# Kernel optimization log

Hardware: AMD Instinct MI355X
Metric: run time of the kernel (lower is better)

## Reference

```python
import jax, jax.numpy as jnp
import numpy as np

N_HEAD = 4
TOP_K = 16


def _layernorm(x, g, b, eps=1e-5):
    mu = jnp.mean(x, axis=-1, keepdims=True)
    var = jnp.var(x, axis=-1, keepdims=True)
    return (x - mu) * jax.lax.rsqrt(var + eps) * g + b


def _gelu_new(x):
    c = np.sqrt(2.0 / np.pi).astype(np.float32)
    return 0.5 * x * (1.0 + jnp.tanh(c * (x + 0.044715 * x ** 3)))


def _l2_normalize(x, eps=1e-12):
    n = jnp.sqrt(jnp.sum(x * x, axis=1, keepdims=True))
    return x / jnp.maximum(n, eps)


def setup_inputs() -> dict:
    key = jax.random.key(0)
    ks = jax.random.split(key, 16)
    B, S, DIN, D, L, P, N = 128, 64, 6, 128, 3, 24, 500000
    sd = 0.02
    inp = {
        "x": jax.random.normal(ks[0], (B, S, DIN), jnp.float32),
        "memory_keys": _l2_normalize(jax.random.normal(ks[1], (N, D), jnp.float32)),
        "memory_values": jax.random.normal(ks[2], (N, P, DIN), jnp.float32),
        "wpe": sd * jax.random.normal(ks[3], (S, D), jnp.float32),
        "w_in": sd * jax.random.normal(ks[4], (DIN, D), jnp.float32),
        "b_in": jnp.zeros((D,), jnp.float32),
        "ln1_g": jnp.ones((L, D), jnp.float32),
        "ln1_b": jnp.zeros((L, D), jnp.float32),
        "attn_w": sd * jax.random.normal(ks[5], (L, D, 3 * D), jnp.float32),
        "attn_b": jnp.zeros((L, 3 * D), jnp.float32),
        "attn_pw": sd * jax.random.normal(ks[6], (L, D, D), jnp.float32),
        "attn_pb": jnp.zeros((L, D), jnp.float32),
        "ln2_g": jnp.ones((L, D), jnp.float32),
        "ln2_b": jnp.zeros((L, D), jnp.float32),
        "fc_w": sd * jax.random.normal(ks[7], (L, D, 4 * D), jnp.float32),
        "fc_b": jnp.zeros((L, 4 * D), jnp.float32),
        "mlp_pw": sd * jax.random.normal(ks[8], (L, 4 * D, D), jnp.float32),
        "mlp_pb": jnp.zeros((L, D), jnp.float32),
        "lnf_g": jnp.ones((D,), jnp.float32),
        "lnf_b": jnp.zeros((D,), jnp.float32),
        "w_out": sd * jax.random.normal(ks[9], (S * D, P * DIN), jnp.float32),
        "b_out": jnp.zeros((P * DIN,), jnp.float32),
        "ret_w1": sd * jax.random.normal(ks[10], (DIN, D), jnp.float32),
        "ret_b1": jnp.zeros((D,), jnp.float32),
        "ret_w2": sd * jax.random.normal(ks[11], (S * D, D), jnp.float32),
        "ret_b2": jnp.zeros((D,), jnp.float32),
        "fusion_weight": jnp.float32(0.5),
    }
    return inp


def _forward(x, memory_keys, memory_values, wpe, w_in, b_in, ln1_g, ln1_b,
             attn_w, attn_b, attn_pw, attn_pb, ln2_g, ln2_b, fc_w, fc_b,
             mlp_pw, mlp_pb, lnf_g, lnf_b, w_out, b_out, ret_w1, ret_b1,
             ret_w2, ret_b2, fusion_weight):
    B, S, DIN = x.shape
    D = w_in.shape[1]
    L = attn_w.shape[0]
    P = memory_values.shape[1]
    hd = D // N_HEAD
    # GPT2 backbone with inputs_embeds (eval mode: dropout = identity)
    h = x @ w_in + b_in + wpe[:S]
    causal = jnp.tril(jnp.ones((S, S), bool))
    neg = jnp.finfo(h.dtype).min
    for l in range(L):
        a = _layernorm(h, ln1_g[l], ln1_b[l])
        qkv = a @ attn_w[l] + attn_b[l]                       # [B,S,3D]
        q, k, v = jnp.split(qkv, 3, axis=-1)
        q = q.reshape(B, S, N_HEAD, hd).transpose(0, 2, 1, 3)  # bhsd
        k = k.reshape(B, S, N_HEAD, hd).transpose(0, 2, 1, 3)
        v = v.reshape(B, S, N_HEAD, hd).transpose(0, 2, 1, 3)
        scores = jnp.einsum('bhqd,bhkd->bhqk', q, k) / np.sqrt(hd).astype(np.float32)
        scores = jnp.where(causal, scores, neg)
        att = jax.nn.softmax(scores, axis=-1)
        o = jnp.einsum('bhqk,bhkd->bhqd', att, v)
        o = o.transpose(0, 2, 1, 3).reshape(B, S, D)
        h = h + o @ attn_pw[l] + attn_pb[l]
        m = _layernorm(h, ln2_g[l], ln2_b[l])
        h = h + _gelu_new(m @ fc_w[l] + fc_b[l]) @ mlp_pw[l] + mlp_pb[l]
    h = _layernorm(h, lnf_g, lnf_b)
    base_pred = (h.reshape(B, S * D) @ w_out + b_out).reshape(B, P, DIN)
    # Retrieval branch: encode query, cosine sim against memory, top-k gather
    q_emb = (x @ ret_w1 + ret_b1).reshape(B, S * D) @ ret_w2 + ret_b2
    q_emb = _l2_normalize(q_emb)
    sim = q_emb @ memory_keys.T                               # [B,N] (memory-bound)
    topk_sim, topk_idx = jax.lax.top_k(sim, TOP_K)
    weights = jax.nn.softmax(topk_sim, axis=1)                # [B,K]
    vals = memory_values[topk_idx]                            # [B,K,P,DIN] gather
    retrieved = jnp.einsum('bk,bkpd->bpd', weights, vals)
    alpha = jax.nn.sigmoid(fusion_weight)
    return alpha * base_pred + (1.0 - alpha) * retrieved


def reference(x, memory_keys, memory_values, wpe, w_in, b_in, ln1_g, ln1_b,
              attn_w, attn_b, attn_pw, attn_pb, ln2_g, ln2_b, fc_w, fc_b,
              mlp_pw, mlp_pb, lnf_g, lnf_b, w_out, b_out, ret_w1, ret_b1,
              ret_w2, ret_b2, fusion_weight):
    return _forward(x, memory_keys, memory_values, wpe, w_in, b_in, ln1_g, ln1_b,
                    attn_w, attn_b, attn_pw, attn_pb, ln2_g, ln2_b, fc_w, fc_b,
                    mlp_pw, mlp_pb, lnf_g, lnf_b, w_out, b_out, ret_w1, ret_b1,
                    ret_w2, ret_b2, fusion_weight)
```

## Files before the change

kernel.cpp:

```cpp
#include <hip/hip_runtime.h>
#include <math.h>

#define TOK   8192
#define DM    128
#define NKEY  500000
#define PDIM  144
#define KSPLIT 128

#define SB     512
#define NPASS  7813
#define NCAND  (SB * 16)

typedef __attribute__((ext_vector_type(8))) short short8;
typedef __attribute__((ext_vector_type(4))) float f32x4;

__device__ __forceinline__ short f2bf(float x) {
    union { float f; unsigned u; } v; v.f = x;
    unsigned r = v.u + 0x7FFFu + ((v.u >> 16) & 1u);
    return (short)(r >> 16);
}
__device__ __forceinline__ float bf2f(short h) {
    union { float f; unsigned u; } v;
    v.u = ((unsigned)(unsigned short)h) << 16;
    return v.f;
}

__device__ __forceinline__ void ins16(float v, int id, float* tv, int* tix) {
#pragma unroll
    for (int j = 15; j > 0; j--) {
        bool up = v > tv[j];
        bool sh = v > tv[j - 1];
        float nv = sh ? tv[j - 1] : v;
        int   ni = sh ? tix[j - 1] : id;
        tv[j]  = up ? nv : tv[j];
        tix[j] = up ? ni : tix[j];
    }
    if (v > tv[0]) { tv[0] = v; tix[0] = id; }
}

__global__ __launch_bounds__(256) void k_embed2(
    const float* __restrict__ x, const float* __restrict__ w,
    const float* __restrict__ b, const float* __restrict__ wpe,
    float* __restrict__ out, const float* __restrict__ rw,
    const float* __restrict__ rb, float* __restrict__ rout)
{
    int bid = blockIdx.x;
    if (bid < 4096) {
        int idx = bid * 256 + threadIdx.x;
        int t = idx >> 7, d = idx & 127;
        float acc = b[d] + wpe[(t & 63) * DM + d];
        const float* xr = x + t * 6;
#pragma unroll
        for (int i = 0; i < 6; i++) acc = fmaf(xr[i], w[i * DM + d], acc);
        out[idx] = acc;
    } else {
        int idx = (bid - 4096) * 256 + threadIdx.x;
        int t = idx >> 7, d = idx & 127;
        float acc = rb[d];
        const float* xr = x + t * 6;
#pragma unroll
        for (int i = 0; i < 6; i++) acc = fmaf(xr[i], rw[i * DM + d], acc);
        rout[idx] = acc;
    }
}

__global__ __launch_bounds__(256) void k_ln(
    const float* __restrict__ in, const float* __restrict__ g,
    const float* __restrict__ b, float* __restrict__ out)
{
    int row = blockIdx.x * 4 + (threadIdx.x >> 6);
    int lane = threadIdx.x & 63;
    const float* r = in + row * DM;
    float v0 = r[lane], v1 = r[lane + 64];
    float s = v0 + v1, ss = v0 * v0 + v1 * v1;
#pragma unroll
    for (int o = 32; o; o >>= 1) { s += __shfl_down(s, o); ss += __shfl_down(ss, o); }
    s = __shfl(s, 0); ss = __shfl(ss, 0);
    float mean = s * (1.f / 128.f);
    float var = ss * (1.f / 128.f) - mean * mean;
    float rstd = rsqrtf(var + 1e-5f);
    out[row * DM + lane]      = (v0 - mean) * rstd * g[lane]      + b[lane];
    out[row * DM + lane + 64] = (v1 - mean) * rstd * g[lane + 64] + b[lane + 64];
}

template<int ACT>
__global__ __launch_bounds__(256) void k_gemmln(
    const float* __restrict__ A, const float* __restrict__ g,
    const float* __restrict__ bln, const float* __restrict__ W,
    const float* __restrict__ bias, float* __restrict__ C, int NC)
{
    __shared__ float As[128][68];
    __shared__ float Ws[16][68];
    const int tid = threadIdx.x;
    const int m0 = blockIdx.x * 64, n0 = blockIdx.y * 64;
    {
        int row = tid >> 2, part = tid & 3;
        const float* ar = A + (long)(m0 + row) * 128 + part * 32;
        float v[32];
        float s = 0.f, ss = 0.f;
#pragma unroll
        for (int i2 = 0; i2 < 8; i2++) {
            float4 t = *(const float4*)(ar + i2 * 4);
            v[i2 * 4 + 0] = t.x; v[i2 * 4 + 1] = t.y;
            v[i2 * 4 + 2] = t.z; v[i2 * 4 + 3] = t.w;
            s += t.x + t.y + t.z + t.w;
            ss += t.x * t.x + t.y * t.y + t.z * t.z + t.w * t.w;
        }
        s += __shfl_xor(s, 1); s += __shfl_xor(s, 2);
        ss += __shfl_xor(ss, 1); ss += __shfl_xor(ss, 2);
        float mean = s * (1.f / 128.f);
        float rstd = rsqrtf(ss * (1.f / 128.f) - mean * mean + 1e-5f);
#pragma unroll
        for (int i = 0; i < 32; i++) {
            int d = part * 32 + i;
            As[d][row] = (v[i] - mean) * rstd * g[d] + bln[d];
        }
    }
    const int ty = tid >> 4, tx = tid & 15;
    float acc[4][4];
#pragma unroll
    for (int i = 0; i < 4; i++)
#pragma unroll
        for (int j = 0; j < 4; j++) acc[i][j] = 0.f;
    __syncthreads();
    for (int k0 = 0; k0 < 128; k0 += 16) {
        {
            int kk = tid >> 4, n = (tid & 15) * 4;
            *(float4*)&Ws[kk][n] = *(const float4*)(W + (long)(k0 + kk) * NC + n0 + n);
        }
        __syncthreads();
#pragma unroll
        for (int kk = 0; kk < 16; kk++) {
            float av[4], wv[4];
            *(float4*)av = *(const float4*)&As[k0 + kk][ty * 4];
            *(float4*)wv = *(const float4*)&Ws[kk][tx * 4];
#pragma unroll
            for (int i = 0; i < 4; i++)
#pragma unroll
                for (int j = 0; j < 4; j++) acc[i][j] = fmaf(av[i], wv[j], acc[i][j]);
        }
        __syncthreads();
    }
#pragma unroll
    for (int i = 0; i < 4; i++) {
        int m = m0 + ty * 4 + i;
#pragma unroll
        for (int j = 0; j < 4; j++) {
            int n = n0 + tx * 4 + j;
            float u = acc[i][j] + bias[n];
            if (ACT) {
                float z = 0.7978845608028654f * (u + 0.044715f * u * u * u);
                z = fminf(fmaxf(z, -15.f), 15.f);
                float t = __expf(2.f * z);
                u = 0.5f * u * (1.f + (t - 1.f) / (t + 1.f));
            }
            C[(long)m * NC + n] = u;
        }
    }
}

template<int KD>
__global__ __launch_bounds__(256) void k_gemm(
    const float* __restrict__ A, const float* __restrict__ W,
    const float* __restrict__ bias, const float* __restrict__ resid,
    float* __restrict__ C, int NC)
{
    __shared__ float As[16][68];
    __shared__ float Ws[16][68];
    const int m0 = blockIdx.x * 64, n0 = blockIdx.y * 64;
    const int tid = threadIdx.x, ty = tid >> 4, tx = tid & 15;
    float acc[4][4];
#pragma unroll
    for (int i = 0; i < 4; i++)
#pragma unroll
        for (int j = 0; j < 4; j++) acc[i][j] = 0.f;
    for (int k0 = 0; k0 < KD; k0 += 16) {
        {
            int m = tid >> 2, kk = (tid & 3) * 4;
            float4 av = *(const float4*)(A + (long)(m0 + m) * KD + k0 + kk);
            As[kk][m] = av.x; As[kk + 1][m] = av.y; As[kk + 2][m] = av.z; As[kk + 3][m] = av.w;
        }
        {
            int kk = tid >> 4, n = (tid & 15) * 4;
            *(float4*)&Ws[kk][n] = *(const float4*)(W + (long)(k0 + kk) * NC + n0 + n);
        }
        __syncthreads();
#pragma unroll
        for (int kk = 0; kk < 16; kk++) {
            float av[4], wv[4];
            *(float4*)av = *(const float4*)&As[kk][ty * 4];
            *(float4*)wv = *(const float4*)&Ws[kk][tx * 4];
#pragma unroll
            for (int i = 0; i < 4; i++)
#pragma unroll
                for (int j = 0; j < 4; j++) acc[i][j] = fmaf(av[i], wv[j], acc[i][j]);
        }
        __syncthreads();
    }
#pragma unroll
    for (int i = 0; i < 4; i++) {
        int m = m0 + ty * 4 + i;
#pragma unroll
        for (int j = 0; j < 4; j++) {
            int n = n0 + tx * 4 + j;
            float u = acc[i][j] + bias[n];
            if (resid) u += resid[(long)m * NC + n];
            C[(long)m * NC + n] = u;
        }
    }
}

__global__ __launch_bounds__(256) void k_attn(
    const float* __restrict__ qkv, float* __restrict__ o)
{
    int b = blockIdx.x >> 2, h = blockIdx.x & 3;
    __shared__ float q[64][33], k[64][33], v[64][33];
    __shared__ float att[64][65];
    int tid = threadIdx.x;
#pragma unroll
    for (int it = 0; it < 8; it++) {
        int idx = it * 256 + tid; int s = idx >> 5, d = idx & 31;
        const float* base = qkv + (long)(b * 64 + s) * 384 + h * 32 + d;
        q[s][d] = base[0]; k[s][d] = base[128]; v[s][d] = base[256];
    }
    __syncthreads();
    {
        int sq = tid >> 2, sk0 = (tid & 3) * 16;
        float e[16]; float mx = -3.0e38f;
#pragma unroll
        for (int j = 0; j < 16; j++) {
            int sk = sk0 + j;
            float a = 0.f;
#pragma unroll
            for (int d = 0; d < 32; d++) a = fmaf(q[sq][d], k[sk][d], a);
            a = (sk <= sq) ? a * 0.17677669529663687f : -3.0e38f;
            e[j] = a; mx = fmaxf(mx, a);
        }
        mx = fmaxf(mx, __shfl_xor(mx, 1)); mx = fmaxf(mx, __shfl_xor(mx, 2));
        float s = 0.f;
#pragma unroll
        for (int j = 0; j < 16; j++) { e[j] = __expf(e[j] - mx); s += e[j]; }
        s += __shfl_xor(s, 1); s += __shfl_xor(s, 2);
        float inv = 1.f / s;
#pragma unroll
        for (int j = 0; j < 16; j++) att[sq][sk0 + j] = e[j] * inv;
    }
    __syncthreads();
#pragma unroll
    for (int it = 0; it < 8; it++) {
        int idx = it * 256 + tid; int s = idx >> 5, d = idx & 31;
        float acc = 0.f;
        for (int sk = 0; sk < 64; sk++) acc = fmaf(att[s][sk], v[sk][d], acc);
        o[(long)(b * 64 + s) * 128 + h * 32 + d] = acc;
    }
}

template<int NC>
__global__ __launch_bounds__(256) void k_head(
    const float* __restrict__ A, const float* __restrict__ W,
    float* __restrict__ part)
{
    constexpr int NPT = NC / 16;
    __shared__ float As[16][132];
    __shared__ float Ws[16][NC + 4];
    const int tid = threadIdx.x, ty = tid >> 4, tx = tid & 15;
    float acc[8][NPT];
#pragma unroll
    for (int i = 0; i < 8; i++)
#pragma unroll
        for (int j = 0; j < NPT; j++) acc[i][j] = 0.f;
    const int kbase = blockIdx.x * 64;
    for (int kc = 0; kc < 4; kc++) {
        int k0 = kbase + kc * 16;
        {
            int m = tid >> 1, kk = (tid & 1) * 8;
            const float* ap = A + (long)m * 8192 + k0 + kk;
            float4 a0 = *(const float4*)ap;
            float4 a1 = *(const float4*)(ap + 4);
            As[kk + 0][m] = a0.x; As[kk + 1][m] = a0.y; As[kk + 2][m] = a0.z; As[kk + 3][m] = a0.w;
            As[kk + 4][m] = a1.x; As[kk + 5][m] = a1.y; As[kk + 6][m] = a1.z; As[kk + 7][m] = a1.w;
        }
        for (int e = tid; e < 16 * NC; e += 256) {
            int kk = e / NC, n = e - kk * NC;
            Ws[kk][n] = W[(long)(k0 + kk) * NC + n];
        }
        __syncthreads();
#pragma unroll
        for (int kk = 0; kk < 16; kk++) {
            float av[8];
            *(float4*)av       = *(const float4*)&As[kk][ty * 8];
            *(float4*)(av + 4) = *(const float4*)&As[kk][ty * 8 + 4];
#pragma unroll
            for (int j = 0; j < NPT; j++) {
                float wv = Ws[kk][tx * NPT + j];
#pragma unroll
                for (int i = 0; i < 8; i++) acc[i][j] = fmaf(av[i], wv, acc[i][j]);
            }
        }
        __syncthreads();
    }
    float* pp = part + (long)blockIdx.x * (128 * NC);
#pragma unroll
    for (int i = 0; i < 8; i++)
#pragma unroll
        for (int j = 0; j < NPT; j++)
            pp[(ty * 8 + i) * NC + tx * NPT + j] = acc[i][j];
}

__global__ __launch_bounds__(256) void k_redhead(
    const float* __restrict__ part, const float* __restrict__ bias,
    float* __restrict__ out, int MN, int NC)
{
    int idx = blockIdx.x * 256 + threadIdx.x;
    if (idx >= MN) return;
    float s = bias[idx % NC];
    for (int b = 0; b < KSPLIT; b++) s += part[(long)b * MN + idx];
    out[idx] = s;
}

__global__ __launch_bounds__(256) void k_redhead_qe(
    const float* __restrict__ part, const float* __restrict__ bias,
    float* __restrict__ out, float* __restrict__ ssq)
{
    __shared__ float hsum[4];
    int tid = threadIdx.x;
    int idx = blockIdx.x * 256 + tid;
    float s = bias[idx & 127];
    for (int b = 0; b < KSPLIT; b++) s += part[(long)b * 16384 + idx];
    out[idx] = s;
    float sq = s * s;
#pragma unroll
    for (int o = 32; o; o >>= 1) sq += __shfl_down(sq, o);
    if ((tid & 63) == 0) hsum[tid >> 6] = sq;
    __syncthreads();
    if (tid == 0)   ssq[blockIdx.x * 2]     = hsum[0] + hsum[1];
    if (tid == 128) ssq[blockIdx.x * 2 + 1] = hsum[2] + hsum[3];
}

__global__ __launch_bounds__(256) void k_qprep(
    const float* __restrict__ qe, const float* __restrict__ ssq,
    short* __restrict__ qfh, short* __restrict__ qfl)
{
    int idx = blockIdx.x * 256 + threadIdx.x;
    int j = idx & 7, lane = (idx >> 3) & 63, t = (idx >> 9) & 7, ks = idx >> 12;
    int n = t * 16 + (lane & 15);
    int d = ks * 32 + (lane >> 4) * 8 + j;
    float inv = 1.f / fmaxf(sqrtf(ssq[n]), 1e-12f);
    float x = qe[n * 128 + d] * inv;
    short h = f2bf(x);
    qfh[idx] = h;
    qfl[idx] = f2bf(x - bf2f(h));
}

__device__ __forceinline__ void cvt8(float4 a, float4 b, int4& hi, int4& lo) {
    float e[8] = {a.x, a.y, a.z, a.w, b.x, b.y, b.z, b.w};
    int h[8], l[8];
#pragma unroll
    for (int i = 0; i < 8; i++) {
        short hh = f2bf(e[i]);
        h[i] = (int)hh & 0xFFFF;
        l[i] = (int)f2bf(e[i] - bf2f(hh)) & 0xFFFF;
    }
    hi.x = h[0] | (h[1] << 16); hi.y = h[2] | (h[3] << 16);
    hi.z = h[4] | (h[5] << 16); hi.w = h[6] | (h[7] << 16);
    lo.x = l[0] | (l[1] << 16); lo.y = l[2] | (l[3] << 16);
    lo.z = l[4] | (l[5] << 16); lo.w = l[6] | (l[7] << 16);
}

__global__ __launch_bounds__(512, 2) void k_sim3(
    const float* __restrict__ keys, const short* __restrict__ qfh,
    const short* __restrict__ qfl,
    float* __restrict__ cval, int* __restrict__ cidx)
{
    __shared__ __align__(16) char sm[67584];
    short* afh = (short*)sm;
    short* afl = (short*)(sm + 16384);
    float* simb = (float*)(sm + 32768);

    const int tid = threadIdx.x;
    const int w = tid >> 6, lane = tid & 63;
    const int quad = lane >> 4, l15 = lane & 15;
    const int qg = w;

    short8 bh[4], bl[4];
    {
        const short8* qfh8 = (const short8*)qfh;
        const short8* qfl8 = (const short8*)qfl;
#pragma unroll
        for (int ks = 0; ks < 4; ks++) {
            int f = (ks * 8 + qg) * 64 + lane;
            bh[ks] = qfh8[f]; bl[ks] = qfl8[f];
        }
    }

    float tv[16]; int tix[16];
#pragma unroll
    for (int j = 0; j < 16; j++) { tv[j] = -3.0e38f; tix[j] = 0; }

    const int r = tid >> 3, o = tid & 7;
    const int mt = r >> 4, rr = r & 15;
    const int L = (o & 3) * 16 + rr;
    const int t8a = mt * 4 + (o >> 2);
    const int t8b = mt * 4 + 2 + (o >> 2);
    short* dha = afh + (t8a * 64 + L) * 8;
    short* dla = afl + (t8a * 64 + L) * 8;
    short* dhb = afh + (t8b * 64 + L) * 8;
    short* dlb = afl + (t8b * 64 + L) * 8;

    const int q_own = l15, kq = quad;
    float* sw = simb + w * 1088;

    float4 R[4];
    int p = blockIdx.x;
    {
        int gk = p * 64 + r;
        const float* kp = keys + (long)gk * 128 + o * 8;
        bool ok = gk < NKEY;
        R[0] = ok ? *(const float4*)kp        : make_float4(0.f,0.f,0.f,0.f);
        R[1] = ok ? *(const float4*)(kp + 4)  : make_float4(0.f,0.f,0.f,0.f);
        R[2] = ok ? *(const float4*)(kp + 64) : make_float4(0.f,0.f,0.f,0.f);
        R[3] = ok ? *(const float4*)(kp + 68) : make_float4(0.f,0.f,0.f,0.f);
    }

    for (; p < NPASS; p += SB) {
        {
            int4 hi, lo;
            cvt8(R[0], R[1], hi, lo);
            *(int4*)dha = hi; *(int4*)dla = lo;
            cvt8(R[2], R[3], hi, lo);
            *(int4*)dhb = hi; *(int4*)dlb = lo;
        }
        {
            int pn = p + SB;
            if (pn < NPASS) {
                int gk = pn * 64 + r;
                const float* kp = keys + (long)gk * 128 + o * 8;
                bool ok = gk < NKEY;
                R[0] = ok ? *(const float4*)kp        : make_float4(0.f,0.f,0.f,0.f);
                R[1] = ok ? *(const float4*)(kp + 4)  : make_float4(0.f,0.f,0.f,0.f);
                R[2] = ok ? *(const float4*)(kp + 64) : make_float4(0.f,0.f,0.f,0.f);
                R[3] = ok ? *(const float4*)(kp + 68) : make_float4(0.f,0.f,0.f,0.f);
            }
        }
        __syncthreads();

        f32x4 acc[4];
#pragma unroll
        for (int m = 0; m < 4; m++) acc[m] = (f32x4){0.f, 0.f, 0.f, 0.f};
        const short8* ah8 = (const short8*)afh;
        const short8* al8 = (const short8*)afl;
#pragma unroll
        for (int ks = 0; ks < 4; ks++) {
            short8 ah[4], al[4];
#pragma unroll
            for (int m = 0; m < 4; m++) {
                int f = (m * 4 + ks) * 64 + lane;
                ah[m] = ah8[f]; al[m] = al8[f];
            }
#pragma unroll
            for (int m = 0; m < 4; m++) {
                acc[m] = __builtin_amdgcn_mfma_f32_16x16x32_bf16(ah[m], bh[ks], acc[m], 0, 0, 0);
                acc[m] = __builtin_amdgcn_mfma_f32_16x16x32_bf16(ah[m], bl[ks], acc[m], 0, 0, 0);
                acc[m] = __builtin_amdgcn_mfma_f32_16x16x32_bf16(al[m], bh[ks], acc[m], 0, 0, 0);
            }
        }
#pragma unroll
        for (int m = 0; m < 4; m++)
#pragma unroll
            for (int r4 = 0; r4 < 4; r4++)
                sw[(m * 16 + quad * 4 + r4) * 17 + l15] = acc[m][r4];
        __syncthreads();

        int limit = NKEY - p * 64;
        float thr = tv[15];
#pragma unroll
        for (int bb = 0; bb < 2; bb++) {
            float vv[8];
#pragma unroll
            for (int i = 0; i < 8; i++) {
                int kk = kq * 16 + bb * 8 + i;
                float vx = sw[kk * 17 + q_own];
                vv[i] = (kk < limit) ? vx : -3.0e38f;
            }
            float mx = fmaxf(fmaxf(fmaxf(vv[0], vv[1]), fmaxf(vv[2], vv[3])),
                             fmaxf(fmaxf(vv[4], vv[5]), fmaxf(vv[6], vv[7])));
            if (mx > thr) {
                int kb = p * 64 + kq * 16 + bb * 8;
#pragma unroll
                for (int i = 0; i < 8; i++)
                    if (vv[i] > thr) { ins16(vv[i], kb + i, tv, tix); thr = tv[15]; }
            }
        }
    }

    __syncthreads();
    float* scv = (float*)sm;
    int*   sci = (int*)(sm + 32768);
    {
        int q = qg * 16 + q_own;
#pragma unroll
        for (int j = 0; j < 16; j++) {
            scv[q * 64 + kq * 16 + j] = tv[j];
            sci[q * 64 + kq * 16 + j] = tix[j];
        }
    }
    __syncthreads();
    if (tid < 128) {
        float fv[16]; int fi[16];
#pragma unroll
        for (int j = 0; j < 16; j++) { fv[j] = -3.0e38f; fi[j] = 0; }
        for (int e = 0; e < 64; e++) {
            float vx = scv[tid * 64 + e];
            if (vx > fv[15]) ins16(vx, sci[tid * 64 + e], fv, fi);
        }
        int ob = (blockIdx.x * 128 + tid) * 16;
#pragma unroll
        for (int j = 0; j < 16; j++) { cval[ob + j] = fv[j]; cidx[ob + j] = fi[j]; }
    }
}

__global__ __launch_bounds__(256) void k_merge(
    const float* __restrict__ cval, const int* __restrict__ cidx,
    const float* __restrict__ base, const float* __restrict__ mvals,
    const float* __restrict__ fw, float* __restrict__ out)
{
    __shared__ float sv[NCAND];
    __shared__ int   si[NCAND];
    __shared__ float wv[4]; __shared__ int wi[4];
    __shared__ float tvs[16]; __shared__ int tis[16];
    const int q = blockIdx.x, tid = threadIdx.x;
    for (int i = tid; i < NCAND; i += 256) {
        sv[i] = cval[(i >> 4) * 2048 + q * 16 + (i & 15)];
        si[i] = cidx[(i >> 4) * 2048 + q * 16 + (i & 15)];
    }
    __syncthreads();
    for (int r = 0; r < 16; r++) {
        float bv = -3.0e38f; int bp = -1;
        for (int i = tid; i < NCAND; i += 256) {
            float v = sv[i];
            if (v > bv) { bv = v; bp = i; }
        }
#pragma unroll
        for (int o = 32; o; o >>= 1) {
            float ov = __shfl_down(bv, o); int op = __shfl_down(bp, o);
            if (ov > bv) { bv = ov; bp = op; }
        }
        if ((tid & 63) == 0) { wv[tid >> 6] = bv; wi[tid >> 6] = bp; }
        __syncthreads();
        if (tid == 0) {
            float b2 = wv[0]; int p2 = wi[0];
            for (int ww = 1; ww < 4; ww++) if (wv[ww] > b2) { b2 = wv[ww]; p2 = wi[ww]; }
            tvs[r] = b2; tis[r] = si[p2]; sv[p2] = -3.0e38f;
        }
        __syncthreads();
    }
    float alpha = 1.f / (1.f + __expf(-fw[0]));
    if (tid < PDIM) {
        float m = tvs[0];
#pragma unroll
        for (int r = 1; r < 16; r++) m = fmaxf(m, tvs[r]);
        float wgt[16]; float s = 0.f;
#pragma unroll
        for (int r = 0; r < 16; r++) { wgt[r] = __expf(tvs[r] - m); s += wgt[r]; }
        float inv = 1.f / s;
        float ret = 0.f;
#pragma unroll
        for (int r = 0; r < 16; r++) ret += wgt[r] * inv * mvals[(long)tis[r] * PDIM + tid];
        out[q * PDIM + tid] = alpha * base[q * PDIM + tid] + (1.f - alpha) * ret;
    }
}

extern "C" void kernel_launch(void* const* d_in, const int* in_sizes, int n_in,
                              void* d_out, int out_size, void* d_ws, size_t ws_size,
                              hipStream_t stream)
{
    const float* x      = (const float*)d_in[0];
    const float* keys   = (const float*)d_in[1];
    const float* mvals  = (const float*)d_in[2];
    const float* wpe    = (const float*)d_in[3];
    const float* w_in   = (const float*)d_in[4];
    const float* b_in   = (const float*)d_in[5];
    const float* ln1_g  = (const float*)d_in[6];
    const float* ln1_b  = (const float*)d_in[7];
    const float* attn_w = (const float*)d_in[8];
    const float* attn_b = (const float*)d_in[9];
    const float* attn_pw= (const float*)d_in[10];
    const float* attn_pb= (const float*)d_in[11];
    const float* ln2_g  = (const float*)d_in[12];
    const float* ln2_b  = (const float*)d_in[13];
    const float* fc_w   = (const float*)d_in[14];
    const float* fc_b   = (const float*)d_in[15];
    const float* mlp_pw = (const float*)d_in[16];
    const float* mlp_pb = (const float*)d_in[17];
    const float* lnf_g  = (const float*)d_in[18];
    const float* lnf_b  = (const float*)d_in[19];
    const float* w_out  = (const float*)d_in[20];
    const float* b_out  = (const float*)d_in[21];
    const float* ret_w1 = (const float*)d_in[22];
    const float* ret_b1 = (const float*)d_in[23];
    const float* ret_w2 = (const float*)d_in[24];
    const float* ret_b2 = (const float*)d_in[25];
    const float* fw     = (const float*)d_in[26];
    float* out = (float*)d_out;

    float* ws   = (float*)d_ws;
    float* h    = ws + 0;
    float* bufA = ws + 1048576;
    float* bufB = ws + 2097152;
    float* bufO = ws + 6291456;
    float* part = ws + 7340032;
    float* base = ws + 9699328;
    float* qe   = ws + 9717760;
    float* ssq  = ws + 9734144;
    short* qfh  = (short*)(ws + 9734272);
    short* qfl  = (short*)(ws + 9742464);
    float* cval = bufB;
    int*   cidx = (int*)part;

    k_embed2<<<8192, 256, 0, stream>>>(x, w_in, b_in, wpe, h, ret_w1, ret_b1, bufO);
    for (int l = 0; l < 3; l++) {
        k_gemmln<0><<<dim3(128, 6), 256, 0, stream>>>(h, ln1_g + l * 128,
            ln1_b + l * 128, attn_w + l * 49152, attn_b + l * 384, bufB, 384);
        k_attn<<<512, 256, 0, stream>>>(bufB, bufA);
        k_gemm<128><<<dim3(128, 2), 256, 0, stream>>>(bufA, attn_pw + l * 16384,
            attn_pb + l * 128, h, h, 128);
        k_gemmln<1><<<dim3(128, 8), 256, 0, stream>>>(h, ln2_g + l * 128,
            ln2_b + l * 128, fc_w + l * 65536, fc_b + l * 512, bufB, 512);
        k_gemm<512><<<dim3(128, 2), 256, 0, stream>>>(bufB, mlp_pw + l * 65536,
            mlp_pb + l * 128, h, h, 128);
    }
    k_ln<<<2048, 256, 0, stream>>>(h, lnf_g, lnf_b, bufA);
    k_head<144><<<KSPLIT, 256, 0, stream>>>(bufA, w_out, part);
    k_redhead<<<72, 256, 0, stream>>>(part, b_out, base, 128 * 144, 144);

    k_head<128><<<KSPLIT, 256, 0, stream>>>(bufO, ret_w2, part);
    k_redhead_qe<<<64, 256, 0, stream>>>(part, ret_b2, qe, ssq);
    k_qprep<<<64, 256, 0, stream>>>(qe, ssq, qfh, qfl);

    k_sim3<<<SB, 512, 0, stream>>>(keys, qfh, qfl, cval, cidx);
    k_merge<<<128, 256, 0, stream>>>(cval, cidx, base, mvals, fw, out);
}
```

Measured before the change: 1.207 ms.

## Use single bf16 similarity pass with fp32 rescoring of top-32 candidates

The similarity kernel drops the bf16 hi/lo split (three MFMAs per tile) and uses one bf16 MFMA. To keep top-k accuracy, the merge kernel now selects 32 candidates per query and recomputes their exact fp32 dot products before picking the final 16. The sim kernel also keeps top-k in registers straight from the accumulators, merges per-lane lists with cross-lane bitonic shuffles instead of shared-memory staging, double-buffers the LDS tile, and raises the occupancy hint. The risk is that bf16 error pushes a true top-16 key outside the 32 shortlisted candidates.

Result: slower. 1.239 ms (+2.6%).

```diff
diff --git a/kernel.cpp b/kernel.cpp
--- a/kernel.cpp
+++ b/kernel.cpp
@@ -18,11 +18,6 @@
     union { float f; unsigned u; } v; v.f = x;
     unsigned r = v.u + 0x7FFFu + ((v.u >> 16) & 1u);
     return (short)(r >> 16);
-}
-__device__ __forceinline__ float bf2f(short h) {
-    union { float f; unsigned u; } v;
-    v.u = ((unsigned)(unsigned short)h) << 16;
-    return v.f;
 }
 
 __device__ __forceinline__ void ins16(float v, int id, float* tv, int* tix) {
@@ -36,6 +31,36 @@
         tix[j] = up ? ni : tix[j];
     }
     if (v > tv[0]) { tv[0] = v; tix[0] = id; }
+}
+
+__device__ __forceinline__ void merge16(float* tv, int* tix, int mask) {
+    float ov[16]; int oi[16];
+#pragma unroll
+    for (int j = 0; j < 16; j++) {
+        ov[j] = __shfl_xor(tv[j], mask);
+        oi[j] = __shfl_xor(tix[j], mask);
+    }
+#pragma unroll
+    for (int j = 0; j < 16; j++) {
+        bool a = tv[j] >= ov[15 - j];
+        float nv = a ? tv[j] : ov[15 - j];
+        int   ni = a ? tix[j] : oi[15 - j];
+        tv[j] = nv; tix[j] = ni;
+    }
+#pragma unroll
+    for (int d = 8; d >= 1; d >>= 1) {
+#pragma unroll
+        for (int j = 0; j < 16; j++) {
+            if ((j & d) == 0) {
+                bool sw = tv[j] < tv[j + d];
+                float a0 = sw ? tv[j + d] : tv[j];
+                float a1 = sw ? tv[j]     : tv[j + d];
+                int   b0 = sw ? tix[j + d] : tix[j];
+                int   b1 = sw ? tix[j]     : tix[j + d];
+                tv[j] = a0; tv[j + d] = a1; tix[j] = b0; tix[j + d] = b1;
+            }
+        }
+    }
 }
 
 __global__ __launch_bounds__(256) void k_embed2(
@@ -339,58 +364,40 @@
 
 __global__ __launch_bounds__(256) void k_qprep(
     const float* __restrict__ qe, const float* __restrict__ ssq,
-    short* __restrict__ qfh, short* __restrict__ qfl)
+    short* __restrict__ qfh)
 {
     int idx = blockIdx.x * 256 + threadIdx.x;
     int j = idx & 7, lane = (idx >> 3) & 63, t = (idx >> 9) & 7, ks = idx >> 12;
     int n = t * 16 + (lane & 15);
     int d = ks * 32 + (lane >> 4) * 8 + j;
     float inv = 1.f / fmaxf(sqrtf(ssq[n]), 1e-12f);
-    float x = qe[n * 128 + d] * inv;
-    short h = f2bf(x);
-    qfh[idx] = h;
-    qfl[idx] = f2bf(x - bf2f(h));
-}
-
-__device__ __forceinline__ void cvt8(float4 a, float4 b, int4& hi, int4& lo) {
+    qfh[idx] = f2bf(qe[n * 128 + d] * inv);
+}
+
+__device__ __forceinline__ void cvt8h(float4 a, float4 b, int4& hi) {
     float e[8] = {a.x, a.y, a.z, a.w, b.x, b.y, b.z, b.w};
-    int h[8], l[8];
-#pragma unroll
-    for (int i = 0; i < 8; i++) {
-        short hh = f2bf(e[i]);
-        h[i] = (int)hh & 0xFFFF;
-        l[i] = (int)f2bf(e[i] - bf2f(hh)) & 0xFFFF;
-    }
+    int h[8];
+#pragma unroll
+    for (int i = 0; i < 8; i++) h[i] = (int)f2bf(e[i]) & 0xFFFF;
     hi.x = h[0] | (h[1] << 16); hi.y = h[2] | (h[3] << 16);
     hi.z = h[4] | (h[5] << 16); hi.w = h[6] | (h[7] << 16);
-    lo.x = l[0] | (l[1] << 16); lo.y = l[2] | (l[3] << 16);
-    lo.z = l[4] | (l[5] << 16); lo.w = l[6] | (l[7] << 16);
-}
-
-__global__ __launch_bounds__(512, 2) void k_sim3(
+}
+
+__global__ __launch_bounds__(512, 4) void k_sim3(
     const float* __restrict__ keys, const short* __restrict__ qfh,
-    const short* __restrict__ qfl,
     float* __restrict__ cval, int* __restrict__ cidx)
 {
-    __shared__ __align__(16) char sm[67584];
-    short* afh = (short*)sm;
-    short* afl = (short*)(sm + 16384);
-    float* simb = (float*)(sm + 32768);
+    __shared__ __align__(16) short afh[2][8192];
 
     const int tid = threadIdx.x;
     const int w = tid >> 6, lane = tid & 63;
     const int quad = lane >> 4, l15 = lane & 15;
-    const int qg = w;
-
-    short8 bh[4], bl[4];
+
+    short8 bh[4];
     {
         const short8* qfh8 = (const short8*)qfh;
-        const short8* qfl8 = (const short8*)qfl;
-#pragma unroll
-        for (int ks = 0; ks < 4; ks++) {
-            int f = (ks * 8 + qg) * 64 + lane;
-            bh[ks] = qfh8[f]; bl[ks] = qfl8[f];
-        }
+#pragma unroll
+        for (int ks = 0; ks < 4; ks++) bh[ks] = qfh8[(ks * 8 + w) * 64 + lane];
     }
 
     float tv[16]; int tix[16];
@@ -400,15 +407,8 @@
     const int r = tid >> 3, o = tid & 7;
     const int mt = r >> 4, rr = r & 15;
     const int L = (o & 3) * 16 + rr;
-    const int t8a = mt * 4 + (o >> 2);
-    const int t8b = mt * 4 + 2 + (o >> 2);
-    short* dha = afh + (t8a * 64 + L) * 8;
-    short* dla = afl + (t8a * 64 + L) * 8;
-    short* dhb = afh + (t8b * 64 + L) * 8;
-    short* dlb = afl + (t8b * 64 + L) * 8;
-
-    const int q_own = l15, kq = quad;
-    float* sw = simb + w * 1088;
+    const int da = ((mt * 4 + (o >> 2)) * 64 + L) * 8;
+    const int db = ((mt * 4 + 2 + (o >> 2)) * 64 + L) * 8;
 
     float4 R[4];
     int p = blockIdx.x;
@@ -422,13 +422,14 @@
         R[3] = ok ? *(const float4*)(kp + 68) : make_float4(0.f,0.f,0.f,0.f);
     }
 
+    int cur = 0;
     for (; p < NPASS; p += SB) {
         {
-            int4 hi, lo;
-            cvt8(R[0], R[1], hi, lo);
-            *(int4*)dha = hi; *(int4*)dla = lo;
-            cvt8(R[2], R[3], hi, lo);
-            *(int4*)dhb = hi; *(int4*)dlb = lo;
+            int4 hi;
+            cvt8h(R[0], R[1], hi);
+            *(int4*)(afh[cur] + da) = hi;
+            cvt8h(R[2], R[3], hi);
+            *(int4*)(afh[cur] + db) = hi;
         }
         {
             int pn = p + SB;
@@ -447,94 +448,68 @@
         f32x4 acc[4];
 #pragma unroll
         for (int m = 0; m < 4; m++) acc[m] = (f32x4){0.f, 0.f, 0.f, 0.f};
-        const short8* ah8 = (const short8*)afh;
-        const short8* al8 = (const short8*)afl;
+        const short8* ah8 = (const short8*)afh[cur];
 #pragma unroll
         for (int ks = 0; ks < 4; ks++) {
-            short8 ah[4], al[4];
-#pragma unroll
-            for (int m = 0; m < 4; m++) {
-                int f = (m * 4 + ks) * 64 + lane;
-                ah[m] = ah8[f]; al[m] = al8[f];
-            }
-#pragma unroll
-            for (int m = 0; m < 4; m++) {
+            short8 ah[4];
+#pragma unroll
+            for (int m = 0; m < 4; m++) ah[m] = ah8[(m * 4 + ks) * 64 + lane];
+#pragma unroll
+            for (int m = 0; m < 4; m++)
                 acc[m] = __builtin_amdgcn_mfma_f32_16x16x32_bf16(ah[m], bh[ks], acc[m], 0, 0, 0);
-                acc[m] = __builtin_amdgcn_mfma_f32_16x16x32_bf16(ah[m], bl[ks], acc[m], 0, 0, 0);
-                acc[m] = __builtin_amdgcn_mfma_f32_16x16x32_bf16(al[m], bh[ks], acc[m], 0, 0, 0);
-            }
-        }
-#pragma unroll
-        for (int m = 0; m < 4; m++)
-#pragma unroll
-            for (int r4 = 0; r4 < 4; r4++)
-                sw[(m * 16 + quad * 4 + r4) * 17 + l15] = acc[m][r4];
-        __syncthreads();
+        }
 
         int limit = NKEY - p * 64;
         float thr = tv[15];
 #pragma unroll
-        for (int bb = 0; bb < 2; bb++) {
-            float vv[8];
-#pragma unroll
-            for (int i = 0; i < 8; i++) {
-                int kk = kq * 16 + bb * 8 + i;
-                float vx = sw[kk * 17 + q_own];
-                vv[i] = (kk < limit) ? vx : -3.0e38f;
+        for (int m = 0; m < 4; m++) {
+            float mx = fmaxf(fmaxf(acc[m][0], acc[m][1]), fmaxf(acc[m][2], acc[m][3]));
+            if (mx > thr) {
+                int kl = m * 16 + quad * 4;
+#pragma unroll
+                for (int r4 = 0; r4 < 4; r4++) {
+                    float v = acc[m][r4];
+                    if (v > thr && (kl + r4) < limit) {
+                        ins16(v, p * 64 + kl + r4, tv, tix);
+                        thr = tv[15];
+                    }
+                }
             }
-            float mx = fmaxf(fmaxf(fmaxf(vv[0], vv[1]), fmaxf(vv[2], vv[3])),
-                             fmaxf(fmaxf(vv[4], vv[5]), fmaxf(vv[6], vv[7])));
-            if (mx > thr) {
-                int kb = p * 64 + kq * 16 + bb * 8;
-#pragma unroll
-                for (int i = 0; i < 8; i++)
-                    if (vv[i] > thr) { ins16(vv[i], kb + i, tv, tix); thr = tv[15]; }
-            }
-        }
-    }
-
-    __syncthreads();
-    float* scv = (float*)sm;
-    int*   sci = (int*)(sm + 32768);
-    {
-        int q = qg * 16 + q_own;
-#pragma unroll
-        for (int j = 0; j < 16; j++) {
-            scv[q * 64 + kq * 16 + j] = tv[j];
-            sci[q * 64 + kq * 16 + j] = tix[j];
-        }
-    }
-    __syncthreads();
-    if (tid < 128) {
-        float fv[16]; int fi[16];
-#pragma unroll
-        for (int j = 0; j < 16; j++) { fv[j] = -3.0e38f; fi[j] = 0; }
-        for (int e = 0; e < 64; e++) {
-            float vx = scv[tid * 64 + e];
-            if (vx > fv[15]) ins16(vx, sci[tid * 64 + e], fv, fi);
-        }
-        int ob = (blockIdx.x * 128 + tid) * 16;
-#pragma unroll
-        for (int j = 0; j < 16; j++) { cval[ob + j] = fv[j]; cidx[ob + j] = fi[j]; }
+        }
+        cur ^= 1;
+    }
+
+    merge16(tv, tix, 16);
+    merge16(tv, tix, 32);
+
+    if (quad == 0) {
+        int q = w * 16 + l15;
+        long ob = ((long)blockIdx.x * 128 + q) * 16;
+#pragma unroll
+        for (int j = 0; j < 16; j++) { cval[ob + j] = tv[j]; cidx[ob + j] = tix[j]; }
     }
 }
 
 __global__ __launch_bounds__(256) void k_merge(
     const float* __restrict__ cval, const int* __restrict__ cidx,
     const float* __restrict__ base, const float* __restrict__ mvals,
-    const float* __restrict__ fw, float* __restrict__ out)
+    const float* __restrict__ fw, const float* __restrict__ keys,
+    const float* __restrict__ qe, const float* __restrict__ ssq,
+    float* __restrict__ out)
 {
     __shared__ float sv[NCAND];
     __shared__ int   si[NCAND];
     __shared__ float wv[4]; __shared__ int wi[4];
-    __shared__ float tvs[16]; __shared__ int tis[16];
+    __shared__ int   tis[32];
+    __shared__ float exv[32];
+    __shared__ float fvs[16]; __shared__ int fis[16];
     const int q = blockIdx.x, tid = threadIdx.x;
     for (int i = tid; i < NCAND; i += 256) {
         sv[i] = cval[(i >> 4) * 2048 + q * 16 + (i & 15)];
         si[i] = cidx[(i >> 4) * 2048 + q * 16 + (i & 15)];
     }
     __syncthreads();
-    for (int r = 0; r < 16; r++) {
+    for (int rsel = 0; rsel < 32; rsel++) {
         float bv = -3.0e38f; int bp = -1;
         for (int i = tid; i < NCAND; i += 256) {
             float v = sv[i];
@@ -550,22 +525,48 @@
         if (tid == 0) {
             float b2 = wv[0]; int p2 = wi[0];
             for (int ww = 1; ww < 4; ww++) if (wv[ww] > b2) { b2 = wv[ww]; p2 = wi[ww]; }
-            tvs[r] = b2; tis[r] = si[p2]; sv[p2] = -3.0e38f;
-        }
-        __syncthreads();
-    }
+            tis[rsel] = si[p2]; sv[p2] = -3.0e38f;
+        }
+        __syncthreads();
+    }
+    {
+        int c = tid >> 3, pp = tid & 7;
+        int idx = tis[c];
+        const float* kr = keys + (long)idx * 128 + pp * 16;
+        const float* qr = qe + q * 128 + pp * 16;
+        float s = 0.f;
+#pragma unroll
+        for (int d2 = 0; d2 < 16; d2++) s = fmaf(qr[d2], kr[d2], s);
+        s += __shfl_xor(s, 1); s += __shfl_xor(s, 2); s += __shfl_xor(s, 4);
+        if (pp == 0) exv[c] = s;
+    }
+    __syncthreads();
+    if (tid < 64) {
+        float inv = 1.f / fmaxf(sqrtf(ssq[q]), 1e-12f);
+        float v = (tid < 32) ? exv[tid] : -3.0e38f;
+        int   id = (tid < 32) ? tis[tid] : -1;
+        for (int rsel = 0; rsel < 16; rsel++) {
+            float bv = v; int bi = id;
+#pragma unroll
+            for (int o = 32; o; o >>= 1) {
+                float ov = __shfl_xor(bv, o); int oi = __shfl_xor(bi, o);
+                if (ov > bv) { bv = ov; bi = oi; }
+            }
+            if (v == bv && id == bi) v = -3.0e38f;
+            if (tid == 0) { fvs[rsel] = bv * inv; fis[rsel] = bi; }
+        }
+    }
+    __syncthreads();
     float alpha = 1.f / (1.f + __expf(-fw[0]));
     if (tid < PDIM) {
-        float m = tvs[0];
-#pragma unroll
-        for (int r = 1; r < 16; r++) m = fmaxf(m, tvs[r]);
+        float m = fvs[0];
         float wgt[16]; float s = 0.f;
 #pragma unroll
-        for (int r = 0; r < 16; r++) { wgt[r] = __expf(tvs[r] - m); s += wgt[r]; }
+        for (int rsel = 0; rsel < 16; rsel++) { wgt[rsel] = __expf(fvs[rsel] - m); s += wgt[rsel]; }
         float inv = 1.f / s;
         float ret = 0.f;
 #pragma unroll
-        for (int r = 0; r < 16; r++) ret += wgt[r] * inv * mvals[(long)tis[r] * PDIM + tid];
+        for (int rsel = 0; rsel < 16; rsel++) ret += wgt[rsel] * inv * mvals[(long)fis[rsel] * PDIM + tid];
         out[q * PDIM + tid] = alpha * base[q * PDIM + tid] + (1.f - alpha) * ret;
     }
 }
@@ -613,7 +614,6 @@
     float* qe   = ws + 9717760;
     float* ssq  = ws + 9734144;
     short* qfh  = (short*)(ws + 9734272);
-    short* qfl  = (short*)(ws + 9742464);
     float* cval = bufB;
     int*   cidx = (int*)part;
 
@@ -635,8 +635,8 @@
 
     k_head<128><<<KSPLIT, 256, 0, stream>>>(bufO, ret_w2, part);
     k_redhead_qe<<<64, 256, 0, stream>>>(part, ret_b2, qe, ssq);
-    k_qprep<<<64, 256, 0, stream>>>(qe, ssq, qfh, qfl);
-
-    k_sim3<<<SB, 512, 0, stream>>>(keys, qfh, qfl, cval, cidx);
-    k_merge<<<128, 256, 0, stream>>>(cval, cidx, base, mvals, fw, out);
-}
+    k_qprep<<<64, 256, 0, stream>>>(qe, ssq, qfh);
+
+    k_sim3<<<SB, 512, 0, stream>>>(keys, qfh, cval, cidx);
+    k_merge<<<128, 256, 0, stream>>>(cval, cidx, base, mvals, fw, keys, qe, ssq, out);
+}
```
